# Kernel optimization log

Measured on AMD Instinct MI355X. Metric: run time of the kernel, lower is better.

Reference implementation:

```python
import jax, jax.numpy as jnp
import numpy as np

K = 3            # attn_kernels
PAD = K // 2
NORM_SCALE = 1.0
EPS = 1e-4


def _conv(x, w, pad):
    # NCHW conv, stride 1, symmetric padding
    return jax.lax.conv_general_dilated(
        x, w, window_strides=(1, 1), padding=[(pad, pad), (pad, pad)],
        dimension_numbers=('NCHW', 'OIHW', 'NCHW'))


def _unfold(x, k, stride, pad):
    # torch.nn.functional.unfold: returns [B, C*k*k, L], feature order (c, kh, kw),
    # L in row-major patch order.
    if pad:
        x = jnp.pad(x, ((0, 0), (0, 0), (pad, pad), (pad, pad)))
    B, C, H, W = x.shape
    oh = (H - k) // stride + 1
    ow = (W - k) // stride + 1
    cols = []
    for i in range(k):          # small fixed k*k loop (k=3)
        for j in range(k):
            cols.append(x[:, :, i:i + stride * (oh - 1) + 1:stride,
                               j:j + stride * (ow - 1) + 1:stride])
    p = jnp.stack(cols, axis=2)             # [B, C, k*k, oh, ow]
    return p.reshape(B, C * k * k, oh * ow)


def setup_inputs() -> dict:
    key = jax.random.key(0)
    k1, k2, k3, k4 = jax.random.split(key, 4)
    B, Cin, Cout, H, W = 8, 192, 192, 96, 96
    fan = Cin * K * K
    x1 = jax.random.normal(k1, (B, Cin, H, W), jnp.float32)
    x2 = jax.random.normal(k2, (B, Cin, H, W), jnp.float32)
    key_w = jax.random.normal(k3, (Cin, Cin, K, K), jnp.float32) / np.sqrt(fan)
    query_w = jax.random.normal(k4, (Cout, Cin, K, K), jnp.float32) / np.sqrt(fan)
    kernel_momentum = jnp.zeros((), jnp.float32)  # init 0.0 as in module
    return {"x1": x1, "x2": x2, "key_w": key_w, "query_w": query_w,
            "kernel_momentum": kernel_momentum}


def reference(x1, x2, key_w, query_w, kernel_momentum):
    B, Cin, H, W = x1.shape
    Cout = query_w.shape[0]
    fk = K * K

    # key: conv then non-overlapping unfold -> [B, fk, Cin, L]
    kf = _unfold(_conv(x1, key_w, PAD), K, stride=K, pad=0)
    L = kf.shape[-1]
    kf = kf.reshape(B, Cin, fk, L).transpose(0, 2, 1, 3)      # [B, fk, Cin, L]

    # query: conv then non-overlapping unfold -> [B, fk, L, Cout]
    qf = _unfold(_conv(x2, query_w, PAD), K, stride=K, pad=0)
    qf = qf.reshape(B, Cout, fk, L).transpose(0, 2, 3, 1)     # [B, fk, L, Cout]

    # attention kernels: [B, fk, Cin, Cout] -> [B, Cout, Cin*fk]
    attn = jnp.einsum('bkcl,bklo->bkco', kf, qf)
    attn = attn.transpose(0, 3, 2, 1).reshape(B, Cout, Cin * fk)

    # custom global mean/std normalization with momentum (torch std is unbiased)
    m = attn.mean()
    s = jnp.std(attn, ddof=1)
    attn = kernel_momentum * attn + NORM_SCALE * (attn - m) / (s + EPS)

    # apply kernels to dense (stride-1, padded) unfold of x1
    v = _unfold(x1, K, stride=1, pad=PAD)                     # [B, Cin*fk, H*W]
    out = jnp.einsum('bcf,bfl->bcl', attn, v)                 # [B, Cout, H*W]
    return out.reshape(B, Cout, H, W)
```

## Files before the change

kernel.cpp:

```cpp
#include <hip/hip_runtime.h>
#include <math.h>

typedef __attribute__((ext_vector_type(8))) short s16x8;
typedef __attribute__((ext_vector_type(4))) short s16x4;
typedef __attribute__((ext_vector_type(4))) float f32x4;

typedef unsigned int u32;
typedef __attribute__((address_space(3))) u32* lds_u32p;
typedef const __attribute__((address_space(1))) u32* glb_u32p;

namespace {

constexpr int B  = 8;
constexpr int C  = 192;
constexpr int H  = 96;
constexpr int W  = 96;
constexpr int FK = 9;
constexpr int HP = 98;
constexpr int L  = 1024;
constexpr int WCHUNK = FK * 12 * 6;
constexpr int WELEM  = WCHUNK * 512;

__device__ inline unsigned short f2b(float f) {
    unsigned int x = __float_as_uint(f);
    x += 0x7fffu + ((x >> 16) & 1u);
    return (unsigned short)(x >> 16);
}

__global__ __launch_bounds__(256) void prep_x(const float* __restrict__ x,
                                              unsigned short* __restrict__ xpadT) {
    __shared__ float xs[192][33];
    const int tid = threadIdx.x;
    const int x0  = blockIdx.x * 32;
    const int y   = blockIdx.y;
    const int b   = blockIdx.z;
    for (int e = tid; e < 192 * 32; e += 256) {
        const int ci = e >> 5, xx = e & 31;
        xs[ci][xx] = x[(((size_t)b * C + ci) * H + y) * W + x0 + xx];
    }
    __syncthreads();
    for (int e = tid; e < 32 * 192; e += 256) {
        const int pos = e / 192, ci = e - pos * 192;
        xpadT[(((size_t)(b * HP + y + 1)) * HP + x0 + pos + 1) * 192 + ci] = f2b(xs[ci][pos]);
    }
}

__global__ __launch_bounds__(256) void prep_w(const float* __restrict__ kw,
                                              const float* __restrict__ qw,
                                              unsigned short* __restrict__ kwA,
                                              unsigned short* __restrict__ qwA) {
    int idx = blockIdx.x * 256 + threadIdx.x;
    const float* src = kw;
    unsigned short* dst = kwA;
    if (idx >= WELEM) { idx -= WELEM; src = qw; dst = qwA; }
    const int chunk = idx >> 9, within = idx & 511;
    const int lane = within >> 3, t = within & 7;
    const int kg = lane >> 4, r15 = lane & 15;
    const int cc = chunk % 6, c2 = chunk / 6;
    const int cot = c2 % 12, p = c2 / 12;
    const int co = cot * 16 + r15;
    const int ci = cc * 32 + kg * 8 + t;
    dst[idx] = f2b(src[((size_t)co * C + ci) * FK + p]);
}

template <bool OUTF32, bool PERB>
__global__ __launch_bounds__(256, 3)
void conv_mfma(const unsigned short* __restrict__ xpadT,
               const unsigned short* __restrict__ wA,
               void* __restrict__ yout) {
    __shared__ __align__(16) char smem[50 * 384];
    const int tid  = threadIdx.x;
    const int y    = blockIdx.x;
    const int sx   = blockIdx.y;
    const int b    = blockIdx.z;
    const int lane = tid & 63, wc = tid >> 6;
    const int ln15 = lane & 15, kg = lane >> 4;

    const unsigned short* wp = PERB ? (wA + (size_t)b * WELEM) : wA;

    int gfull[4];
#pragma unroll
    for (int it = 0; it < 4; ++it) {
        const int m = it * 256 + tid;
        const int q = m / 24, c16 = m - q * 24;
        gfull[it] = (sx * 48 + q) * 384 + ((c16 * 16) ^ ((q & 7) << 4));
    }
    int gtail = 0;
    if (tid < 176) {
        const int m = 1024 + tid;
        const int q = m / 24, c16 = m - q * 24;
        gtail = (sx * 48 + q) * 384 + ((c16 * 16) ^ ((q & 7) << 4));
    }

    auto stage = [&](int prow) {
        const char* rowbase = (const char*)(xpadT + ((size_t)(b * HP + prow)) * HP * 192);
#pragma unroll
        for (int it = 0; it < 4; ++it)
            __builtin_amdgcn_global_load_lds(
                (glb_u32p)(const void*)(rowbase + gfull[it]),
                (lds_u32p)(void*)(smem + it * 4096 + wc * 1024), 16, 0, 0);
        if (tid < 176)
            __builtin_amdgcn_global_load_lds(
                (glb_u32p)(const void*)(rowbase + gtail),
                (lds_u32p)(void*)(smem + 16384 + wc * 1024), 16, 0, 0);
    };

    f32x4 acc[3][3];
#pragma unroll
    for (int i = 0; i < 3; ++i)
#pragma unroll
        for (int j = 0; j < 3; ++j)
            acc[i][j] = (f32x4){0.f, 0.f, 0.f, 0.f};

    for (int dy = 0; dy < 3; ++dy) {
        if (dy) __syncthreads();
        stage(y + dy);
        asm volatile("s_waitcnt vmcnt(0)" ::: "memory");
        __syncthreads();

        for (int cc = 0; cc < 6; ++cc) {
            s16x8 af[3][3];
#pragma unroll
            for (int dx = 0; dx < 3; ++dx)
#pragma unroll
                for (int i = 0; i < 3; ++i) {
                    const int chunkid = ((3 * dy + dx) * 12 + wc * 3 + i) * 6 + cc;
                    af[dx][i] = *(const s16x8*)(wp + (size_t)chunkid * 512 + lane * 8);
                }
            s16x8 bv[3][3];
#pragma unroll
            for (int j = 0; j < 3; ++j)
#pragma unroll
                for (int dx = 0; dx < 3; ++dx) {
                    const int q = j * 16 + ln15 + dx;
                    bv[j][dx] = *(const s16x8*)(smem + q * 384 +
                                    ((cc * 64 + kg * 16) ^ ((q & 7) << 4)));
                }
#pragma unroll
            for (int i = 0; i < 3; ++i)
#pragma unroll
                for (int j = 0; j < 3; ++j)
#pragma unroll
                    for (int dx = 0; dx < 3; ++dx)
                        acc[i][j] = __builtin_amdgcn_mfma_f32_16x16x32_bf16(
                            af[dx][i], bv[j][dx], acc[i][j], 0, 0, 0);
        }
    }

    if (!OUTF32) {
        unsigned short* yb = (unsigned short*)yout;
        const int ph = y % 3, lh = y / 3;
        int poff[3];
#pragma unroll
        for (int j = 0; j < 3; ++j) {
            const int s  = sx * 48 + j * 16 + ln15;
            const int pw = s % 3, lw = s / 3;
            poff[j] = ((b * FK + ph * 3 + pw) * C) * L + lh * 32 + lw;
        }
#pragma unroll
        for (int i = 0; i < 3; ++i)
#pragma unroll
            for (int rr = 0; rr < 4; ++rr) {
                const int co = wc * 48 + i * 16 + kg * 4 + rr;
#pragma unroll
                for (int j = 0; j < 3; ++j)
                    yb[(size_t)poff[j] + co * L] = f2b(acc[i][j][rr]);
            }
    } else {
        float* yf = (float*)yout;
#pragma unroll
        for (int i = 0; i < 3; ++i)
#pragma unroll
            for (int rr = 0; rr < 4; ++rr) {
                const int co = wc * 48 + i * 16 + kg * 4 + rr;
                const size_t base = (((size_t)b * C + co) * H + y) * W;
#pragma unroll
                for (int j = 0; j < 3; ++j)
                    yf[base + sx * 48 + j * 16 + ln15] = acc[i][j][rr];
            }
    }
}

__global__ __launch_bounds__(256, 3)
void attn_mfma(const unsigned short* __restrict__ kcS,
               const unsigned short* __restrict__ qcS,
               float* __restrict__ attnT,
               double* __restrict__ part) {
    __shared__ __align__(16) char smem[2][24576];
    const int tid  = threadIdx.x;
    const int lane = tid & 63, wid = tid >> 6;
    const int wq   = wid & 1, wp = wid >> 1;
    const int ln15 = lane & 15, kg = lane >> 4;
    const int of   = blockIdx.x & 1, cf = blockIdx.x >> 1;
    const int p    = blockIdx.y, b = blockIdx.z;

    const char* Abase = (const char*)(kcS + ((size_t)(b * FK + p) * C + cf * 96) * L);
    const char* Bbase = (const char*)(qcS + ((size_t)(b * FK + p) * C + of * 96) * L);

    int gofs[3];
#pragma unroll
    for (int it = 0; it < 3; ++it) {
        const int chunk = it * 256 + tid;
        const int row = chunk >> 3, c16 = chunk & 7;
        gofs[it] = row * 2048 + ((c16 * 16) ^ ((row & 7) << 4));
    }

    auto stage = [&](int bufi, int t) {
        const char* Ab = Abase + t * 128;
        const char* Bb = Bbase + t * 128;
        char* lb = (char*)smem[bufi];
#pragma unroll
        for (int it = 0; it < 3; ++it)
            __builtin_amdgcn_global_load_lds(
                (glb_u32p)(const void*)(Ab + gofs[it]),
                (lds_u32p)(void*)(lb + it * 4096 + wid * 1024), 16, 0, 0);
#pragma unroll
        for (int it = 0; it < 3; ++it)
            __builtin_amdgcn_global_load_lds(
                (glb_u32p)(const void*)(Bb + gofs[it]),
                (lds_u32p)(void*)(lb + 12288 + it * 4096 + wid * 1024), 16, 0, 0);
    };

    f32x4 acc[3][3];
#pragma unroll
    for (int i = 0; i < 3; ++i)
#pragma unroll
        for (int j = 0; j < 3; ++j)
            acc[i][j] = (f32x4){0.f, 0.f, 0.f, 0.f};

    stage(0, 0);
    asm volatile("s_waitcnt vmcnt(0)" ::: "memory");
    __syncthreads();

    for (int t = 0; t < 16; ++t) {
        if (t < 15) stage((t + 1) & 1, t + 1);
        const char* lb = (const char*)smem[t & 1];
#pragma unroll
        for (int ks = 0; ks < 2; ++ks) {
            s16x8 af[3], bf[3];
#pragma unroll
            for (int i = 0; i < 3; ++i) {
                const int row = wp * 48 + i * 16 + ln15;
                af[i] = *(const s16x8*)(lb + row * 128 +
                                        ((ks * 64 + kg * 16) ^ ((row & 7) << 4)));
            }
#pragma unroll
            for (int j = 0; j < 3; ++j) {
                const int row = wq * 48 + j * 16 + ln15;
                bf[j] = *(const s16x8*)(lb + 12288 + row * 128 +
                                        ((ks * 64 + kg * 16) ^ ((row & 7) << 4)));
            }
#pragma unroll
            for (int i = 0; i < 3; ++i)
#pragma unroll
                for (int j = 0; j < 3; ++j)
                    acc[i][j] = __builtin_amdgcn_mfma_f32_16x16x32_bf16(
                        af[i], bf[j], acc[i][j], 0, 0, 0);
        }
        if (t < 15) {
            asm volatile("s_waitcnt vmcnt(0)" ::: "memory");
            __syncthreads();
        }
    }

    __syncthreads();
    double s = 0.0, ss = 0.0;
#pragma unroll
    for (int i = 0; i < 3; ++i)
#pragma unroll
        for (int j = 0; j < 3; ++j)
#pragma unroll
            for (int r = 0; r < 4; ++r) {
                const double v = (double)acc[i][j][r];
                s += v; ss += v * v;
            }
    double* ls  = (double*)&smem[0][0];
    double* lss = ls + 256;
    ls[tid] = s; lss[tid] = ss;
    __syncthreads();
    for (int st = 128; st; st >>= 1) {
        if (tid < st) { ls[tid] += ls[tid + st]; lss[tid] += lss[tid + st]; }
        __syncthreads();
    }
    if (tid == 0) {
        const int bf_ = ((b * FK + p) << 2) + blockIdx.x;
        part[2 * bf_]     = ls[0];
        part[2 * bf_ + 1] = lss[0];
    }

    float* ap = attnT + (size_t)(b * FK + p) * C * C;
#pragma unroll
    for (int i = 0; i < 3; ++i) {
        const int c0 = cf * 96 + wp * 48 + i * 16 + kg * 4;
#pragma unroll
        for (int j = 0; j < 3; ++j) {
            const int o = of * 96 + wq * 48 + j * 16 + ln15;
            *(f32x4*)(ap + o * C + c0) = acc[i][j];
        }
    }
}

__global__ __launch_bounds__(256) void finalize_k(const double* __restrict__ part,
                                                  const float* __restrict__ momp,
                                                  float* __restrict__ scal) {
    __shared__ double ls[256], lss[256];
    double s = 0.0, ss = 0.0;
    for (int i = threadIdx.x; i < 288; i += 256) {
        s += part[2 * i]; ss += part[2 * i + 1];
    }
    ls[threadIdx.x] = s; lss[threadIdx.x] = ss;
    __syncthreads();
    for (int st = 128; st; st >>= 1) {
        if (threadIdx.x < st) {
            ls[threadIdx.x]  += ls[threadIdx.x + st];
            lss[threadIdx.x] += lss[threadIdx.x + st];
        }
        __syncthreads();
    }
    if (threadIdx.x == 0) {
        const double n    = (double)(B * FK * C * C);
        const double mean = ls[0] / n;
        double var        = (lss[0] - ls[0] * ls[0] / n) / (n - 1.0);
        if (var < 0.0) var = 0.0;
        const double scale = 1.0 / (sqrt(var) + 1e-4);
        scal[0] = (float)((double)momp[0] + scale);
        scal[1] = (float)(-mean * scale);
    }
}

__global__ __launch_bounds__(256) void norm_w(const float* __restrict__ attnT,
                                              const float* __restrict__ scal,
                                              unsigned short* __restrict__ o) {
    const float alpha = scal[0], beta = scal[1];
    const int g = (blockIdx.x * 256 + threadIdx.x) * 4;
    const int chunk = g >> 9, within = g & 511;
    const int lane = within >> 3, t0 = within & 7;
    const int cc = chunk % 6, c2 = chunk / 6;
    const int cot = c2 % 12, pb = c2 / 12;
    const int p = pb % FK, b = pb / FK;
    const int co = cot * 16 + (lane & 15);
    const int ci = cc * 32 + (lane >> 4) * 8 + t0;
    const float4 v = *(const float4*)(attnT + (((size_t)(b * FK + p) * C + co) * C + ci));
    s16x4 r;
    r[0] = (short)f2b(fmaf(alpha, v.x, beta));
    r[1] = (short)f2b(fmaf(alpha, v.y, beta));
    r[2] = (short)f2b(fmaf(alpha, v.z, beta));
    r[3] = (short)f2b(fmaf(alpha, v.w, beta));
    *(s16x4*)(o + g) = r;
}

}

extern "C" void kernel_launch(void* const* d_in, const int* in_sizes, int n_in,
                              void* d_out, int out_size, void* d_ws, size_t ws_size,
                              hipStream_t stream) {
    (void)in_sizes; (void)n_in; (void)out_size; (void)ws_size;
    const float* x1   = (const float*)d_in[0];
    const float* x2   = (const float*)d_in[1];
    const float* kw   = (const float*)d_in[2];
    const float* qw   = (const float*)d_in[3];
    const float* momp = (const float*)d_in[4];

    char* ws = (char*)d_ws;
    unsigned short* xpad1 = (unsigned short*)ws;
    unsigned short* xpad2 = (unsigned short*)(ws + 29503488);
    unsigned short* kwA   = (unsigned short*)(ws + 59006976);
    unsigned short* qwA   = (unsigned short*)(ws + 59670528);
    unsigned short* kcS   = (unsigned short*)(ws + 60334080);
    float*          attnT = (float*)(ws + 88645632);
    double*         part  = (double*)(ws + 99262464);
    float*          scal  = (float*)(ws + 99278848);
    unsigned short* normW = kcS;
    unsigned short* qcS   = (unsigned short*)d_out;

    hipMemsetAsync(xpad1, 0, 2 * 29503488ULL, stream);

    dim3 pgrid(3, 96, 8);
    prep_x<<<pgrid, 256, 0, stream>>>(x1, xpad1);
    prep_x<<<pgrid, 256, 0, stream>>>(x2, xpad2);
    prep_w<<<2592, 256, 0, stream>>>(kw, qw, kwA, qwA);

    dim3 cgrid(96, 2, 8);
    conv_mfma<false, false><<<cgrid, 256, 0, stream>>>(xpad1, kwA, kcS);
    conv_mfma<false, false><<<cgrid, 256, 0, stream>>>(xpad2, qwA, qcS);

    attn_mfma<<<dim3(4, 9, 8), 256, 0, stream>>>(kcS, qcS, attnT, part);
    finalize_k<<<1, 256, 0, stream>>>(part, momp, scal);

    norm_w<<<2592, 256, 0, stream>>>(attnT, scal, normW);
    conv_mfma<true, true><<<cgrid, 256, 0, stream>>>(xpad1, normW, (float*)d_out);
}
```

Measured before the change: 284.5 us.

## Double-buffer conv row staging, merge dual convs and prep launches, zero only borders

The conv kernel now holds two LDS row buffers and issues the async global-to-LDS load for the next input row during the last channel chunk of the current row. This overlaps staging with MFMA work and drops one barrier per row. The key and query convolutions are merged into one launch with a doubled grid, as are the two prep_x launches. The full memset of both padded buffers is replaced by a small kernel that zeroes only the border pixels. The risks are higher LDS use per block, with launch bounds raised to 4 blocks per CU, and more register pressure from fully unrolling the cc loop.

```diff
diff --git a/kernel.cpp b/kernel.cpp
--- a/kernel.cpp
+++ b/kernel.cpp
@@ -20,6 +20,7 @@
 constexpr int L  = 1024;
 constexpr int WCHUNK = FK * 12 * 6;
 constexpr int WELEM  = WCHUNK * 512;
+constexpr size_t XPAD_ELEMS = (size_t)B * HP * HP * 192;
 
 __device__ inline unsigned short f2b(float f) {
     unsigned int x = __float_as_uint(f);
@@ -27,13 +28,32 @@
     return (unsigned short)(x >> 16);
 }
 
-__global__ __launch_bounds__(256) void prep_x(const float* __restrict__ x,
+__global__ __launch_bounds__(256) void border_zero(unsigned short* __restrict__ xpad) {
+    const int c   = blockIdx.x * 256 + threadIdx.x;
+    const int c16 = c % 24;
+    const int p_  = c / 24;
+    const int pos = p_ % 388;
+    const int bt  = p_ / 388;
+    int yy, xx;
+    if (pos < 98)       { yy = 0;          xx = pos; }
+    else if (pos < 196) { yy = 97;         xx = pos - 98; }
+    else if (pos < 292) { yy = pos - 195;  xx = 0; }
+    else                { yy = pos - 291;  xx = 97; }
+    const size_t off = (((size_t)bt * HP + yy) * HP + xx) * 192 + c16 * 8;
+    *(s16x8*)(xpad + off) = (s16x8){0, 0, 0, 0, 0, 0, 0, 0};
+}
+
+__global__ __launch_bounds__(256) void prep_x(const float* __restrict__ x1,
+                                              const float* __restrict__ x2,
                                               unsigned short* __restrict__ xpadT) {
     __shared__ float xs[192][33];
     const int tid = threadIdx.x;
     const int x0  = blockIdx.x * 32;
     const int y   = blockIdx.y;
-    const int b   = blockIdx.z;
+    const int zz  = blockIdx.z;
+    const int b   = zz & 7, t = zz >> 3;
+    const float* x = t ? x2 : x1;
+    unsigned short* dst = xpadT + (size_t)t * XPAD_ELEMS;
     for (int e = tid; e < 192 * 32; e += 256) {
         const int ci = e >> 5, xx = e & 31;
         xs[ci][xx] = x[(((size_t)b * C + ci) * H + y) * W + x0 + xx];
@@ -41,7 +61,7 @@
     __syncthreads();
     for (int e = tid; e < 32 * 192; e += 256) {
         const int pos = e / 192, ci = e - pos * 192;
-        xpadT[(((size_t)(b * HP + y + 1)) * HP + x0 + pos + 1) * 192 + ci] = f2b(xs[ci][pos]);
+        dst[(((size_t)(b * HP + y + 1)) * HP + x0 + pos + 1) * 192 + ci] = f2b(xs[ci][pos]);
     }
 }
 
@@ -63,20 +83,28 @@
     dst[idx] = f2b(src[((size_t)co * C + ci) * FK + p]);
 }
 
-template <bool OUTF32, bool PERB>
-__global__ __launch_bounds__(256, 3)
-void conv_mfma(const unsigned short* __restrict__ xpadT,
+template <bool OUTF32, bool PERB, bool DUAL>
+__global__ __launch_bounds__(256, 4)
+void conv_mfma(const unsigned short* __restrict__ xpadA,
+               const unsigned short* __restrict__ xpadB,
                const unsigned short* __restrict__ wA,
-               void* __restrict__ yout) {
-    __shared__ __align__(16) char smem[50 * 384];
+               const unsigned short* __restrict__ wB,
+               void* __restrict__ youtA,
+               void* __restrict__ youtB) {
+    __shared__ __align__(16) char smem[2][19200];
     const int tid  = threadIdx.x;
     const int y    = blockIdx.x;
     const int sx   = blockIdx.y;
-    const int b    = blockIdx.z;
+    const int zz   = blockIdx.z;
+    const int b    = DUAL ? (zz & 7) : zz;
+    const int t    = DUAL ? (zz >> 3) : 0;
+    const unsigned short* xpadT = (DUAL && t) ? xpadB : xpadA;
+    const unsigned short* wbase = (DUAL && t) ? wB : wA;
+    void* yout = (DUAL && t) ? youtB : youtA;
     const int lane = tid & 63, wc = tid >> 6;
     const int ln15 = lane & 15, kg = lane >> 4;
 
-    const unsigned short* wp = PERB ? (wA + (size_t)b * WELEM) : wA;
+    const unsigned short* wp = PERB ? (wbase + (size_t)b * WELEM) : wbase;
 
     int gfull[4];
 #pragma unroll
@@ -92,17 +120,17 @@
         gtail = (sx * 48 + q) * 384 + ((c16 * 16) ^ ((q & 7) << 4));
     }
 
-    auto stage = [&](int prow) {
+    auto stage = [&](char* lb, int prow) {
         const char* rowbase = (const char*)(xpadT + ((size_t)(b * HP + prow)) * HP * 192);
 #pragma unroll
         for (int it = 0; it < 4; ++it)
             __builtin_amdgcn_global_load_lds(
                 (glb_u32p)(const void*)(rowbase + gfull[it]),
-                (lds_u32p)(void*)(smem + it * 4096 + wc * 1024), 16, 0, 0);
+                (lds_u32p)(void*)(lb + it * 4096 + wc * 1024), 16, 0, 0);
         if (tid < 176)
             __builtin_amdgcn_global_load_lds(
                 (glb_u32p)(const void*)(rowbase + gtail),
-                (lds_u32p)(void*)(smem + 16384 + wc * 1024), 16, 0, 0);
+                (lds_u32p)(void*)(lb + 16384 + wc * 1024), 16, 0, 0);
     };
 
     f32x4 acc[3][3];
@@ -112,12 +140,14 @@
         for (int j = 0; j < 3; ++j)
             acc[i][j] = (f32x4){0.f, 0.f, 0.f, 0.f};
 
+    stage(smem[0], y);
+
     for (int dy = 0; dy < 3; ++dy) {
-        if (dy) __syncthreads();
-        stage(y + dy);
         asm volatile("s_waitcnt vmcnt(0)" ::: "memory");
         __syncthreads();
-
+        const char* lb = smem[dy & 1];
+
+#pragma unroll
         for (int cc = 0; cc < 6; ++cc) {
             s16x8 af[3][3];
 #pragma unroll
@@ -127,13 +157,18 @@
                     const int chunkid = ((3 * dy + dx) * 12 + wc * 3 + i) * 6 + cc;
                     af[dx][i] = *(const s16x8*)(wp + (size_t)chunkid * 512 + lane * 8);
                 }
+            if (cc == 5) {
+                __builtin_amdgcn_sched_barrier(0);
+                if (dy < 2) stage((char*)smem[(dy + 1) & 1], y + dy + 1);
+                __builtin_amdgcn_sched_barrier(0);
+            }
             s16x8 bv[3][3];
 #pragma unroll
             for (int j = 0; j < 3; ++j)
 #pragma unroll
                 for (int dx = 0; dx < 3; ++dx) {
                     const int q = j * 16 + ln15 + dx;
-                    bv[j][dx] = *(const s16x8*)(smem + q * 384 +
+                    bv[j][dx] = *(const s16x8*)(lb + q * 384 +
                                     ((cc * 64 + kg * 16) ^ ((q & 7) << 4)));
                 }
 #pragma unroll
@@ -373,20 +408,18 @@
     unsigned short* normW = kcS;
     unsigned short* qcS   = (unsigned short*)d_out;
 
-    hipMemsetAsync(xpad1, 0, 2 * 29503488ULL, stream);
-
-    dim3 pgrid(3, 96, 8);
-    prep_x<<<pgrid, 256, 0, stream>>>(x1, xpad1);
-    prep_x<<<pgrid, 256, 0, stream>>>(x2, xpad2);
+    border_zero<<<582, 256, 0, stream>>>(xpad1);
+
+    prep_x<<<dim3(3, 96, 16), 256, 0, stream>>>(x1, x2, xpad1);
     prep_w<<<2592, 256, 0, stream>>>(kw, qw, kwA, qwA);
 
-    dim3 cgrid(96, 2, 8);
-    conv_mfma<false, false><<<cgrid, 256, 0, stream>>>(xpad1, kwA, kcS);
-    conv_mfma<false, false><<<cgrid, 256, 0, stream>>>(xpad2, qwA, qcS);
+    conv_mfma<false, false, true><<<dim3(96, 2, 16), 256, 0, stream>>>(
+        xpad1, xpad2, kwA, qwA, kcS, qcS);
 
     attn_mfma<<<dim3(4, 9, 8), 256, 0, stream>>>(kcS, qcS, attnT, part);
     finalize_k<<<1, 256, 0, stream>>>(part, momp, scal);
 
     norm_w<<<2592, 256, 0, stream>>>(attnT, scal, normW);
-    conv_mfma<true, true><<<cgrid, 256, 0, stream>>>(xpad1, normW, (float*)d_out);
-}
+    conv_mfma<true, true, false><<<dim3(96, 2, 8), 256, 0, stream>>>(
+        xpad1, nullptr, normW, nullptr, (float*)d_out, nullptr);
+}
```

Measured after the change: 411.3 us. 44.6% more time.
